# Performance work log

Measured on AMD Instinct MI355X. Metric: run time of the kernel, lower is better.

Reference implementation:

```python
import jax, jax.numpy as jnp
import numpy as np

B, C, T, H = 64, 800, 512, 1024
IN = 2 * C  # 1600, matches hardcoded input_size in PCLSTMCell


def setup_inputs() -> dict:
    key = jax.random.key(0)
    ks = jax.random.split(key, 24)
    s = 0.02
    d = {}
    d["x"] = jax.random.normal(ks[0], (B, C, T), jnp.float32)
    d["y"] = jax.random.normal(ks[1], (B, C, T), jnp.float32)
    d["subject_id"] = jax.random.normal(ks[2], (B, 87), jnp.float32)
    for n_i, n in enumerate(["f", "i", "u", "o"]):
        d[f"W_{n}x"] = jax.random.normal(ks[3 + 4 * n_i], (IN, H), jnp.float32) * s
        d[f"b_{n}x"] = jnp.zeros((H,), jnp.float32)
        d[f"W_{n}h"] = jax.random.normal(ks[4 + 4 * n_i], (H, H), jnp.float32) * s
        d[f"b_{n}h"] = jnp.zeros((H,), jnp.float32)
    d["W_init"] = jax.random.normal(ks[20], (87, H), jnp.float32) * s
    d["b_init"] = jnp.zeros((H,), jnp.float32)
    return d


def reference(x, y, subject_id,
              W_fx, b_fx, W_fh, b_fh,
              W_ix, b_ix, W_ih, b_ih,
              W_ux, b_ux, W_uh, b_uh,
              W_ox, b_ox, W_oh, b_oh,
              W_init, b_init):
    Bc, Cc, Tc = x.shape
    Hc = W_fh.shape[0]
    # y_prev[t] = y[t-1], zeros at t=0 (matches torch.zeros at t==0)
    y_prev = jnp.concatenate([jnp.zeros_like(y[..., :1]), y[..., :-1]], axis=-1)
    # torch.stack((x_i, y_prev), dim=-1).view(B,-1): channel-interleaved [x0,y0,x1,y1,...]
    xs = jnp.stack([x, y_prev], axis=2)                    # [B, C, 2, T]
    xs = jnp.moveaxis(xs, -1, 0).reshape(Tc, Bc, 2 * Cc)    # [T, B, 2C]
    # fuse the 4 input-side gate GEMMs and precompute over all timesteps
    Wx = jnp.concatenate([W_fx, W_ix, W_ux, W_ox], axis=1)  # [2C, 4H]
    bx = jnp.concatenate([b_fx, b_ix, b_ux, b_ox])          # [4H]
    gx = jnp.einsum('tbi,ig->tbg', xs, Wx) + bx             # [T, B, 4H]
    Wh = jnp.concatenate([W_fh, W_ih, W_uh, W_oh], axis=1)  # [H, 4H]
    bh = jnp.concatenate([b_fh, b_ih, b_uh, b_oh])

    h0 = jnp.zeros((Bc, Hc), x.dtype)
    c0 = subject_id @ W_init + b_init                       # initilaizer(subject_id)

    def step(carry, gx_t):
        h, c = carry
        g = gx_t + h @ Wh + bh
        f, i, u, o = jnp.split(g, 4, axis=-1)
        f = jax.nn.sigmoid(f)
        i = jax.nn.sigmoid(i)
        u = jnp.tanh(u)
        o = jax.nn.sigmoid(o)
        c = c * f + i * u
        h = o * jnp.tanh(c)
        return (h, c), h

    (_, c_fin), hs = jax.lax.scan(step, (h0, c0), gx)       # hs: [T, B, H]
    h_seq = jnp.moveaxis(hs, 0, -1)                          # [B, H, T]
    return h_seq, c_fin
```

## Files before the change

kernel.cpp:

```cpp
#include <hip/hip_runtime.h>

typedef __attribute__((ext_vector_type(8))) short short8;
typedef __attribute__((ext_vector_type(4))) float f32x4;
typedef __attribute__((ext_vector_type(4))) _Float16 f16x4;
typedef __attribute__((ext_vector_type(4))) unsigned int u32x4;
typedef unsigned long long u64_t;

#define DI __device__ __forceinline__

DI unsigned short f2bf(float f) {
  unsigned int u = __float_as_uint(f);
  u += 0x7FFFu + ((u >> 16) & 1u);
  return (unsigned short)(u >> 16);
}

DI void gload_lds16(const void* g, void* l) {
  __builtin_amdgcn_global_load_lds(
      (const __attribute__((address_space(1))) unsigned int*)g,
      (__attribute__((address_space(3))) unsigned int*)l, 16, 0, 0);
}

DI float sigm(float x) { return 1.f / (1.f + __expf(-x)); }
DI float tanh_(float x) { return 1.f - 2.f / (__expf(2.f * x) + 1.f); }

DI u32x4 h_load16(const void* p) {
  u32x4 r;
  asm volatile("global_load_dwordx4 %0, %1, off sc0 sc1" : "=v"(r) : "v"(p) : "memory");
  return r;
}

static constexpr size_t OFF_WXT  = 0;
static constexpr size_t OFF_WHT  = 13107200;
static constexpr size_t OFF_BSUM = OFF_WHT + 8388608;
static constexpr size_t OFF_XS   = OFF_BSUM + 16384;
static constexpr size_t OFF_GX   = OFF_XS + 104857600;
static constexpr size_t OFF_HBUF = OFF_GX + 268435456;
static constexpr size_t OFF_BAR  = OFF_HBUF + 262144;
static constexpr size_t WS_NEED  = OFF_BAR + 32768;

__global__ __launch_bounds__(256) void pack_w(
    const float* __restrict__ s0, const float* __restrict__ s1,
    const float* __restrict__ s2, const float* __restrict__ s3,
    unsigned short* __restrict__ dst, int K) {
  __shared__ float tile[32][33];
  const int tx = threadIdx.x & 31, ty = threadIdx.x >> 5;
  const int kt = blockIdx.x, nt = blockIdx.y;
  const int q = (nt * 32) >> 10;
  const float* src = (q == 0) ? s0 : (q == 1) ? s1 : (q == 2) ? s2 : s3;
  const int cbase = (nt * 32) & 1023;
#pragma unroll
  for (int i = 0; i < 4; ++i) {
    int k = kt * 32 + ty + i * 8;
    tile[ty + i * 8][tx] = src[(size_t)k * 1024 + cbase + tx];
  }
  __syncthreads();
#pragma unroll
  for (int i = 0; i < 4; ++i) {
    int n = nt * 32 + ty + i * 8;
    dst[(size_t)n * K + kt * 32 + tx] = f2bf(tile[tx][ty + i * 8]);
  }
}

__global__ __launch_bounds__(256) void pack_bias(
    const float* bx0, const float* bx1, const float* bx2, const float* bx3,
    const float* bh0, const float* bh1, const float* bh2, const float* bh3,
    float* __restrict__ bsum) {
  int n = blockIdx.x * 256 + threadIdx.x;
  int q = n >> 10, j = n & 1023;
  const float* bx = (q == 0) ? bx0 : (q == 1) ? bx1 : (q == 2) ? bx2 : bx3;
  const float* bh = (q == 0) ? bh0 : (q == 1) ? bh1 : (q == 2) ? bh2 : bh3;
  bsum[n] = bx[j] + bh[j];
}

__global__ __launch_bounds__(256) void xs_pack(
    const float* __restrict__ x, const float* __restrict__ y,
    unsigned int* __restrict__ xs32) {
  __shared__ float xt[32][33], yt[32][33];
  const int tx = threadIdx.x & 31, ty = threadIdx.x >> 5;
  const int tt = blockIdx.x, ct = blockIdx.y, b = blockIdx.z;
#pragma unroll
  for (int i = 0; i < 4; ++i) {
    int c = ct * 32 + ty + i * 8;
    int t = tt * 32 + tx;
    size_t base = ((size_t)b * 800 + c) * 512;
    xt[ty + i * 8][tx] = x[base + t];
    yt[ty + i * 8][tx] = (t == 0) ? 0.f : y[base + t - 1];
  }
  __syncthreads();
#pragma unroll
  for (int i = 0; i < 4; ++i) {
    int t = tt * 32 + ty + i * 8;
    int c = ct * 32 + tx;
    unsigned int pk = ((unsigned int)f2bf(yt[tx][ty + i * 8]) << 16) |
                      (unsigned int)f2bf(xt[tx][ty + i * 8]);
    xs32[((size_t)t * 64 + b) * 800 + c] = pk;
  }
}

__global__ __launch_bounds__(256, 2) void gemm_gx(
    const unsigned short* __restrict__ xs, const unsigned short* __restrict__ Wxt,
    const float* __restrict__ bsum, _Float16* __restrict__ gx) {
  __shared__ __align__(16) unsigned short Al[128 * 64];
  __shared__ __align__(16) unsigned short Bl[128 * 64];
  const int tid = threadIdx.x;
  const int w = tid >> 6, l = tid & 63;
  const int l15 = l & 15, l4 = l >> 4;
  const int wm = w >> 1, wn = w & 1;
  const int u = (blockIdx.x & 7) * 1024 + (blockIdx.x >> 3);
  const int bm = u >> 5, bn = u & 31;

  f32x4 acc[4][4];
#pragma unroll
  for (int i = 0; i < 4; ++i)
#pragma unroll
    for (int j = 0; j < 4; ++j) acc[i][j] = (f32x4){0.f, 0.f, 0.f, 0.f};

  const int srow = w * 8 + (l >> 3);
  const int scol = (l & 7) * 8;

  for (int kt = 0; kt < 25; ++kt) {
#pragma unroll
    for (int rnd = 0; rnd < 4; ++rnd) {
      int row = rnd * 32 + srow;
      gload_lds16(xs + ((size_t)(bm * 128 + row)) * 1600 + kt * 64 + scol,
                  Al + rnd * 2048 + w * 512);
      gload_lds16(Wxt + ((size_t)(bn * 128 + row)) * 1600 + kt * 64 + scol,
                  Bl + rnd * 2048 + w * 512);
    }
    __syncthreads();
#pragma unroll
    for (int kk = 0; kk < 64; kk += 32) {
      short8 av[4], bv[4];
#pragma unroll
      for (int mf = 0; mf < 4; ++mf)
        av[mf] = *(const short8*)&Al[(wm * 64 + mf * 16 + l15) * 64 + kk + l4 * 8];
#pragma unroll
      for (int nf = 0; nf < 4; ++nf)
        bv[nf] = *(const short8*)&Bl[(wn * 64 + nf * 16 + l15) * 64 + kk + l4 * 8];
#pragma unroll
      for (int mf = 0; mf < 4; ++mf)
#pragma unroll
        for (int nf = 0; nf < 4; ++nf)
          acc[mf][nf] = __builtin_amdgcn_mfma_f32_16x16x32_bf16(
              av[mf], bv[nf], acc[mf][nf], 0, 0, 0);
    }
    __syncthreads();
  }
#pragma unroll
  for (int nf = 0; nf < 4; ++nf) {
    int col = bn * 128 + wn * 64 + nf * 16 + l15;
    float bs = bsum[col];
    int colp = (col & 1023) * 4 + (col >> 10);
#pragma unroll
    for (int mf = 0; mf < 4; ++mf) {
      int row0 = bm * 128 + wm * 64 + mf * 16 + l4 * 4;
#pragma unroll
      for (int j = 0; j < 4; ++j)
        gx[(size_t)(row0 + j) * 4096 + colp] = (_Float16)(acc[mf][nf][j] + bs);
    }
  }
}

__global__ __launch_bounds__(512, 2) void lstm_seq(
    const _Float16* __restrict__ gx, const unsigned short* __restrict__ Wht,
    const float* __restrict__ subj, const float* __restrict__ Winit,
    const float* __restrict__ binit, float* __restrict__ out,
    unsigned int* __restrict__ hbuf, unsigned int* __restrict__ bar) {
  const int gg  = blockIdx.x & 7;
  const int cwg = blockIdx.x >> 3;
  const int tid = threadIdx.x;
  const int w = tid >> 6, l = tid & 63;
  const int l15 = l & 15, l4 = l >> 4;
  const int ws = w & 1, kq = w >> 1;
  const int ghc = cwg * 32 + ws * 16 + l15;

  __shared__ __align__(16) char smem[98304];

  short8 Bf[32];
  {
    const unsigned short* wp =
        Wht + (size_t)(cwg * 32 + ws * 16 + l15) * 1024 + kq * 256 + l4 * 8;
#pragma unroll
    for (int g = 0; g < 4; ++g)
#pragma unroll
      for (int ks = 0; ks < 8; ++ks)
        Bf[g * 8 + ks] = *(const short8*)(wp + (size_t)g * 1048576 + ks * 32);
  }

  float c[4], hq[4][8];
  if (w < 2 && l4 < 2) {
#pragma unroll
    for (int j = 0; j < 4; ++j) {
      int b = gg * 8 + l4 * 4 + j;
      float a = binit[ghc];
      for (int k = 0; k < 87; ++k) a += subj[b * 87 + k] * Winit[k * 1024 + ghc];
      c[j] = a;
    }
  }

  unsigned int* flags = bar + gg * 1024;

  const int so0 = tid * 16;
  const int so1 = (tid + 512) * 16;
  const int sw0 = so0 ^ (((so0 >> 11) & 7) << 4);
  const int sw1 = so1 ^ (((so1 >> 11) & 7) << 4);

  for (int t8 = 0; t8 < 64; ++t8) {
#pragma unroll
    for (int s = 0; s < 8; ++s) {
      const int t = t8 * 8 + s;
      const int cur = s & 1, nxt = cur ^ 1;
      if (w == 7) {
        const unsigned tgt = (unsigned)t;
        for (;;) {
          unsigned f = 0xFFFFFFFFu;
          if (l < 32)
            f = __hip_atomic_load(flags + l * 32, __ATOMIC_RELAXED,
                                  __HIP_MEMORY_SCOPE_AGENT);
          if (__all(f >= tgt)) break;
          __builtin_amdgcn_s_sleep(1);
        }
      }
      __syncthreads();
      {
        const char* src = (const char*)hbuf + (size_t)(gg * 2 + cur) * 16384;
        u32x4 v0 = h_load16(src + so0);
        u32x4 v1 = h_load16(src + so1);
        asm volatile("s_waitcnt vmcnt(0)" ::: "memory");
        *(u32x4*)(smem + sw0) = v0;
        *(u32x4*)(smem + sw1) = v1;
      }
      f16x4 gxq[4];
      if (w < 2 && l4 < 2) {
        const _Float16* gp =
            gx + ((size_t)(t * 64 + gg * 8 + l4 * 4)) * 4096 + ghc * 4;
#pragma unroll
        for (int j = 0; j < 4; ++j) gxq[j] = *(const f16x4*)(gp + (size_t)j * 4096);
      }
      __syncthreads();
      f32x4 acc[4];
#pragma unroll
      for (int g = 0; g < 4; ++g) acc[g] = (f32x4){0.f, 0.f, 0.f, 0.f};
#pragma unroll
      for (int ks = 0; ks < 8; ++ks) {
        short8 a = *(const short8*)(
            smem + (((l15 & 7) * 2048 + kq * 512 + ks * 64 + l4 * 16) ^ ((l15 & 7) << 4)));
#pragma unroll
        for (int g = 0; g < 4; ++g)
          acc[g] = __builtin_amdgcn_mfma_f32_16x16x32_bf16(a, Bf[g * 8 + ks], acc[g], 0, 0, 0);
      }
      if (w >= 2) {
        char* pb = smem + 16384 + (size_t)(ws * 3 + kq - 1) * 4096;
#pragma unroll
        for (int g = 0; g < 4; ++g) *(f32x4*)(pb + g * 1024 + l * 16) = acc[g];
      }
      __syncthreads();
      if (w < 2) {
        f32x4 red[4];
#pragma unroll
        for (int g = 0; g < 4; ++g) {
          red[g] = acc[g];
#pragma unroll
          for (int kk = 0; kk < 3; ++kk)
            red[g] += *(const f32x4*)(smem + 16384 + (size_t)(ws * 3 + kk) * 4096 +
                                      g * 1024 + l * 16);
        }
        if (l4 < 2) {
#pragma unroll
          for (int j = 0; j < 4; ++j) {
            float fv = sigm(red[0][j] + (float)gxq[j][0]);
            float iv = sigm(red[1][j] + (float)gxq[j][1]);
            float uv = tanh_(red[2][j] + (float)gxq[j][2]);
            float ov = sigm(red[3][j] + (float)gxq[j][3]);
            c[j] = c[j] * fv + iv * uv;
            float hv = ov * tanh_(c[j]);
            hq[j][s] = hv;
            float hn = __shfl_xor(hv, 1);
            if (!(l15 & 1)) {
              unsigned int pk = (unsigned int)f2bf(hv) | ((unsigned int)f2bf(hn) << 16);
              __hip_atomic_store(
                  hbuf + (gg * 2 + nxt) * 4096 + (l4 * 4 + j) * 512 +
                      cwg * 16 + ws * 8 + (l15 >> 1),
                  pk, __ATOMIC_RELAXED, __HIP_MEMORY_SCOPE_AGENT);
            }
          }
        }
      }
      asm volatile("s_waitcnt vmcnt(0)" ::: "memory");
      __syncthreads();
      if (tid == 0)
        __hip_atomic_store(flags + cwg * 32, (unsigned)(t + 1),
                           __ATOMIC_RELAXED, __HIP_MEMORY_SCOPE_AGENT);
    }
    if (w < 2 && l4 < 2) {
      int tb = t8 * 8;
#pragma unroll
      for (int j = 0; j < 4; ++j) {
        f32x4 v0 = {hq[j][0], hq[j][1], hq[j][2], hq[j][3]};
        f32x4 v1 = {hq[j][4], hq[j][5], hq[j][6], hq[j][7]};
        float* op = out + (size_t)(gg * 8 + l4 * 4 + j) * 524288 + (size_t)ghc * 512 + tb;
        *(f32x4*)op = v0;
        *(f32x4*)(op + 4) = v1;
      }
    }
  }
  if (w < 2 && l4 < 2) {
#pragma unroll
    for (int j = 0; j < 4; ++j)
      out[33554432 + (size_t)(gg * 8 + l4 * 4 + j) * 1024 + ghc] = c[j];
  }
}

extern "C" void kernel_launch(void* const* d_in, const int* in_sizes, int n_in,
                              void* d_out, int out_size, void* d_ws, size_t ws_size,
                              hipStream_t stream) {
  (void)in_sizes; (void)n_in; (void)out_size;
  if (ws_size < WS_NEED) return;

  const float* x     = (const float*)d_in[0];
  const float* y     = (const float*)d_in[1];
  const float* subj  = (const float*)d_in[2];
  const float* W_fx  = (const float*)d_in[3];
  const float* b_fx  = (const float*)d_in[4];
  const float* W_fh  = (const float*)d_in[5];
  const float* b_fh  = (const float*)d_in[6];
  const float* W_ix  = (const float*)d_in[7];
  const float* b_ix  = (const float*)d_in[8];
  const float* W_ih  = (const float*)d_in[9];
  const float* b_ih  = (const float*)d_in[10];
  const float* W_ux  = (const float*)d_in[11];
  const float* b_ux  = (const float*)d_in[12];
  const float* W_uh  = (const float*)d_in[13];
  const float* b_uh  = (const float*)d_in[14];
  const float* W_ox  = (const float*)d_in[15];
  const float* b_ox  = (const float*)d_in[16];
  const float* W_oh  = (const float*)d_in[17];
  const float* b_oh  = (const float*)d_in[18];
  const float* Winit = (const float*)d_in[19];
  const float* binit = (const float*)d_in[20];
  float* out = (float*)d_out;

  char* ws = (char*)d_ws;
  unsigned short* Wxt  = (unsigned short*)(ws + OFF_WXT);
  unsigned short* Wht  = (unsigned short*)(ws + OFF_WHT);
  float*          bsum = (float*)(ws + OFF_BSUM);
  unsigned int*   xs32 = (unsigned int*)(ws + OFF_XS);
  _Float16*       gx   = (_Float16*)(ws + OFF_GX);
  unsigned int*   hbuf = (unsigned int*)(ws + OFF_HBUF);
  unsigned int*   bar  = (unsigned int*)(ws + OFF_BAR);

  hipMemsetAsync(ws + OFF_HBUF, 0, WS_NEED - OFF_HBUF, stream);

  pack_w<<<dim3(50, 128), 256, 0, stream>>>(W_fx, W_ix, W_ux, W_ox, Wxt, 1600);
  pack_w<<<dim3(32, 128), 256, 0, stream>>>(W_fh, W_ih, W_uh, W_oh, Wht, 1024);
  pack_bias<<<16, 256, 0, stream>>>(b_fx, b_ix, b_ux, b_ox, b_fh, b_ih, b_uh, b_oh, bsum);
  xs_pack<<<dim3(16, 25, 64), 256, 0, stream>>>(x, y, xs32);
  gemm_gx<<<8192, 256, 0, stream>>>((const unsigned short*)xs32, Wxt, bsum, gx);

  const _Float16* gxc = gx;
  const unsigned short* whtc = Wht;
  void* ka[8] = {(void*)&gxc, (void*)&whtc, (void*)&subj, (void*)&Winit,
                 (void*)&binit, (void*)&out, (void*)&hbuf, (void*)&bar};
  hipError_t e = hipLaunchCooperativeKernel((const void*)lstm_seq, dim3(256), dim3(512),
                                            ka, 0, stream);
  if (e != hipSuccess) {
    lstm_seq<<<256, 512, 0, stream>>>(gxc, whtc, subj, Winit, binit, out, hbuf, bar);
  }
}
```

Measured before the change: 2.786 ms.

## Rewrite input GEMM with 256x256 tiles and triple-buffered async LDS pipeline

The input-projection GEMM moves from 128x128 tiles with single-buffered loads to 256x256 tiles on 512-thread blocks. It uses a three-slot LDS ring with K-step 32 and prefetches three stages ahead under explicit vmcnt waits. Raw s_barrier replaces __syncthreads, and MFMA priority is raised while the matrix ops run. The aim is to overlap global-to-LDS loads with MFMA work and raise arithmetic intensity per block. The cost is 96KB of LDS and a larger accumulator register set, which may limit occupancy.

After: 2.704 ms. -2.9%, faster.

```diff
diff --git a/kernel.cpp b/kernel.cpp
--- a/kernel.cpp
+++ b/kernel.cpp
@@ -97,63 +97,90 @@
   }
 }
 
-__global__ __launch_bounds__(256, 2) void gemm_gx(
+__global__ __launch_bounds__(512, 2) void gemm_gx(
     const unsigned short* __restrict__ xs, const unsigned short* __restrict__ Wxt,
     const float* __restrict__ bsum, _Float16* __restrict__ gx) {
-  __shared__ __align__(16) unsigned short Al[128 * 64];
-  __shared__ __align__(16) unsigned short Bl[128 * 64];
+  __shared__ __align__(16) char smem[98304];
   const int tid = threadIdx.x;
   const int w = tid >> 6, l = tid & 63;
   const int l15 = l & 15, l4 = l >> 4;
-  const int wm = w >> 1, wn = w & 1;
-  const int u = (blockIdx.x & 7) * 1024 + (blockIdx.x >> 3);
-  const int bm = u >> 5, bn = u & 31;
-
-  f32x4 acc[4][4];
-#pragma unroll
-  for (int i = 0; i < 4; ++i)
+  const int wm = w >> 2, wn = w & 3;
+  const int u = (blockIdx.x & 7) * 256 + (blockIdx.x >> 3);
+  const int bm = u >> 4, bn = u & 15;
+
+  const unsigned short* abase0 = xs + (size_t)(bm * 256) * 1600;
+  const unsigned short* bbase0 = Wxt + (size_t)(bn * 256) * 1600;
+
+  const int c0 = w * 64 + l;
+  const int r0 = c0 >> 2, k0 = c0 & 3;
+  const int c1 = 512 + c0;
+  const int r1 = c1 >> 2, k1 = c1 & 3;
+  const int dst0 = w * 1024;
+  const int dst1 = 8192 + w * 1024;
+
+#define STAGE(kt2, slot)                                                        \
+  {                                                                             \
+    const unsigned short* ab = abase0 + (kt2) * 32;                             \
+    const unsigned short* bb = bbase0 + (kt2) * 32;                             \
+    char* Asl = smem + (slot) * 16384;                                          \
+    char* Bsl = smem + 49152 + (slot) * 16384;                                  \
+    gload_lds16(ab + (size_t)r0 * 1600 + k0 * 8, Asl + dst0);                   \
+    gload_lds16(bb + (size_t)r0 * 1600 + k0 * 8, Bsl + dst0);                   \
+    gload_lds16(ab + (size_t)r1 * 1600 + k1 * 8, Asl + dst1);                   \
+    gload_lds16(bb + (size_t)r1 * 1600 + k1 * 8, Bsl + dst1);                   \
+  }
+
+  f32x4 acc[8][4];
+#pragma unroll
+  for (int i = 0; i < 8; ++i)
 #pragma unroll
     for (int j = 0; j < 4; ++j) acc[i][j] = (f32x4){0.f, 0.f, 0.f, 0.f};
 
-  const int srow = w * 8 + (l >> 3);
-  const int scol = (l & 7) * 8;
-
-  for (int kt = 0; kt < 25; ++kt) {
-#pragma unroll
-    for (int rnd = 0; rnd < 4; ++rnd) {
-      int row = rnd * 32 + srow;
-      gload_lds16(xs + ((size_t)(bm * 128 + row)) * 1600 + kt * 64 + scol,
-                  Al + rnd * 2048 + w * 512);
-      gload_lds16(Wxt + ((size_t)(bn * 128 + row)) * 1600 + kt * 64 + scol,
-                  Bl + rnd * 2048 + w * 512);
-    }
-    __syncthreads();
-#pragma unroll
-    for (int kk = 0; kk < 64; kk += 32) {
-      short8 av[4], bv[4];
-#pragma unroll
-      for (int mf = 0; mf < 4; ++mf)
-        av[mf] = *(const short8*)&Al[(wm * 64 + mf * 16 + l15) * 64 + kk + l4 * 8];
+  STAGE(0, 0);
+  STAGE(1, 1);
+  STAGE(2, 2);
+
+  int slot = 0;
+  for (int t = 0; t < 50; ++t) {
+    if (t < 48) {
+      asm volatile("s_waitcnt vmcnt(8)" ::: "memory");
+    } else {
+      asm volatile("s_waitcnt vmcnt(0)" ::: "memory");
+    }
+    __builtin_amdgcn_s_barrier();
+    const char* Asl = smem + slot * 16384;
+    const char* Bsl = smem + 49152 + slot * 16384;
+    short8 af[8], bf[4];
+#pragma unroll
+    for (int mf = 0; mf < 8; ++mf)
+      af[mf] = *(const short8*)(Asl + (wm * 128 + mf * 16 + l15) * 64 + l4 * 16);
+#pragma unroll
+    for (int nf = 0; nf < 4; ++nf)
+      bf[nf] = *(const short8*)(Bsl + (wn * 64 + nf * 16 + l15) * 64 + l4 * 16);
+    asm volatile("s_waitcnt lgkmcnt(0)" ::: "memory");
+    __builtin_amdgcn_sched_barrier(0);
+    __builtin_amdgcn_s_barrier();
+    if (t + 3 < 50) STAGE(t + 3, slot);
+    __builtin_amdgcn_s_setprio(1);
+#pragma unroll
+    for (int mf = 0; mf < 8; ++mf)
 #pragma unroll
       for (int nf = 0; nf < 4; ++nf)
-        bv[nf] = *(const short8*)&Bl[(wn * 64 + nf * 16 + l15) * 64 + kk + l4 * 8];
-#pragma unroll
-      for (int mf = 0; mf < 4; ++mf)
-#pragma unroll
-        for (int nf = 0; nf < 4; ++nf)
-          acc[mf][nf] = __builtin_amdgcn_mfma_f32_16x16x32_bf16(
-              av[mf], bv[nf], acc[mf][nf], 0, 0, 0);
-    }
-    __syncthreads();
-  }
+        acc[mf][nf] = __builtin_amdgcn_mfma_f32_16x16x32_bf16(
+            af[mf], bf[nf], acc[mf][nf], 0, 0, 0);
+    __builtin_amdgcn_s_setprio(0);
+    slot = (slot == 2) ? 0 : slot + 1;
+  }
+#undef STAGE
+
 #pragma unroll
   for (int nf = 0; nf < 4; ++nf) {
-    int col = bn * 128 + wn * 64 + nf * 16 + l15;
+    int col = bn * 256 + wn * 64 + nf * 16 + l15;
     float bs = bsum[col];
     int colp = (col & 1023) * 4 + (col >> 10);
 #pragma unroll
-    for (int mf = 0; mf < 4; ++mf) {
-      int row0 = bm * 128 + wm * 64 + mf * 16 + l4 * 4;
+    for (int mf = 0; mf < 8; ++mf) {
+      int row0 = bm * 256 + wm * 128 + mf * 16 + l4 * 4;
 #pragma unroll
       for (int j = 0; j < 4; ++j)
         gx[(size_t)(row0 + j) * 4096 + colp] = (_Float16)(acc[mf][nf][j] + bs);
@@ -355,7 +382,7 @@
   pack_w<<<dim3(32, 128), 256, 0, stream>>>(W_fh, W_ih, W_uh, W_oh, Wht, 1024);
   pack_bias<<<16, 256, 0, stream>>>(b_fx, b_ix, b_ux, b_ox, b_fh, b_ih, b_uh, b_oh, bsum);
   xs_pack<<<dim3(16, 25, 64), 256, 0, stream>>>(x, y, xs32);
-  gemm_gx<<<8192, 256, 0, stream>>>((const unsigned short*)xs32, Wxt, bsum, gx);
+  gemm_gx<<<2048, 512, 0, stream>>>((const unsigned short*)xs32, Wxt, bsum, gx);
 
   const _Float16* gxc = gx;
   const unsigned short* whtc = Wht;
```
